# Optimization experiments

Measured on AMD Instinct MI355X. Metric: run time of the kernel, lower is better.

Reference implementation:

```python
import jax, jax.numpy as jnp
import numpy as np

B, T, D, K = 4, 4096, 1024, 64


def setup_inputs() -> dict:
    key = jax.random.key(0)
    k1, k2, k3, k4 = jax.random.split(key, 4)
    x = jax.random.normal(k1, (B, T, D), dtype=jnp.float32)
    Wq = jax.random.normal(k2, (D, K), dtype=jnp.float32) * (D ** -0.5)
    Wk = jax.random.normal(k3, (D, K), dtype=jnp.float32) * (D ** -0.5)
    Wv = jax.random.normal(k4, (D, D), dtype=jnp.float32) * (D ** -0.5)
    return {"x": x, "Wq": Wq, "Wk": Wk, "Wv": Wv}


def reference(x, Wq, Wk, Wv):
    # x: (B,T,D); single-head causal self-attention with value dim = D
    Bx, Tx, Dx = x.shape
    head_size = Wq.shape[-1]
    q = jnp.einsum('btd,dk->btk', x, Wq)  # (B,T,K)
    k = jnp.einsum('btd,dk->btk', x, Wk)  # (B,T,K)
    v = jnp.einsum('btd,de->bte', x, Wv)  # (B,T,D)
    scores = jnp.einsum('bqk,bsk->bqs', q, k) * (head_size ** -0.5)  # (B,T,T)
    causal = jnp.tril(jnp.ones((Tx, Tx), dtype=bool))
    scores = jnp.where(causal[None, :, :], scores, -jnp.inf)
    attn = jax.nn.softmax(scores, axis=-1)
    return jnp.einsum('bqs,bsd->bqd', attn, v)  # (B,T,D)
```

## Files before the change

### kernel.cpp

```cpp
#include <hip/hip_runtime.h>
#include <hip/hip_bf16.h>

typedef __attribute__((ext_vector_type(8))) short bf16x8;
typedef __attribute__((ext_vector_type(4))) float f32x4;
typedef unsigned short u16;

#define MFMA16(a, b, c) __builtin_amdgcn_mfma_f32_16x16x32_bf16((a), (b), (c), 0, 0, 0)
#define GLLDS(gp, lp)                                                                  \
  __builtin_amdgcn_global_load_lds((const __attribute__((address_space(1))) unsigned int*)(gp), \
                                   (__attribute__((address_space(3))) unsigned int*)(lp), 16, 0, 0)

__device__ __forceinline__ u16 f2b(float f) {
  union { float f; unsigned u; } x; x.f = f;
  return (u16)((x.u + 0x7FFFu + ((x.u >> 16) & 1u)) >> 16);
}
__device__ __forceinline__ u16 f2b_hw(float f) {
  union { __hip_bfloat16 h; u16 u; } c;
  c.h = __float2bfloat16(f);
  return c.u;
}

__global__ __launch_bounds__(256) void k_cvt(const float* __restrict__ in,
                                             u16* __restrict__ out, int n4) {
  int i = blockIdx.x * 256 + threadIdx.x;
  if (i >= n4) return;
  float4 v = ((const float4*)in)[i];
  u16 a = f2b(v.x), b = f2b(v.y), c = f2b(v.z), d = f2b(v.w);
  ((uint2*)out)[i] = make_uint2((unsigned)a | ((unsigned)b << 16),
                                (unsigned)c | ((unsigned)d << 16));
}

__global__ __launch_bounds__(256) void k_packT(const float* __restrict__ in,
                                               u16* __restrict__ out, int R, int C) {
  __shared__ float t[32][33];
  int r0 = blockIdx.x * 32, c0 = blockIdx.y * 32;
  int cx = threadIdx.x & 31, ry = threadIdx.x >> 5;
#pragma unroll
  for (int k = 0; k < 4; k++)
    t[ry + k * 8][cx] = in[(size_t)(r0 + ry + k * 8) * C + c0 + cx];
  __syncthreads();
#pragma unroll
  for (int k = 0; k < 4; k++)
    out[(size_t)(c0 + ry + k * 8) * R + r0 + cx] = f2b(t[cx][ry + k * 8]);
}

__global__ __launch_bounds__(256) void k_gemm_qk(const u16* __restrict__ xb,
                                                 const u16* __restrict__ wqt,
                                                 const u16* __restrict__ wkt,
                                                 u16* __restrict__ q, u16* __restrict__ kk) {
  int row0 = blockIdx.x * 64;
  int tid = threadIdx.x, w = tid >> 6, l = tid & 63, l15 = l & 15, lg = l >> 4;
  const u16* wt = (w < 2) ? wqt : wkt;
  int nbase = (w & 1) * 32;
  f32x4 acc[4][2];
#pragma unroll
  for (int mt = 0; mt < 4; mt++)
#pragma unroll
    for (int nt = 0; nt < 2; nt++) acc[mt][nt] = (f32x4){0.f, 0.f, 0.f, 0.f};

  for (int k0 = 0; k0 < 1024; k0 += 32) {
    bf16x8 bfr[2], afr[4];
#pragma unroll
    for (int nt = 0; nt < 2; nt++)
      bfr[nt] = *(const bf16x8*)&wt[(size_t)(nbase + nt * 16 + l15) * 1024 + k0 + lg * 8];
#pragma unroll
    for (int mt = 0; mt < 4; mt++)
      afr[mt] = *(const bf16x8*)&xb[(size_t)(row0 + mt * 16 + l15) * 1024 + k0 + lg * 8];
#pragma unroll
    for (int mt = 0; mt < 4; mt++)
#pragma unroll
      for (int nt = 0; nt < 2; nt++) acc[mt][nt] = MFMA16(afr[mt], bfr[nt], acc[mt][nt]);
  }
  if (w < 2) {
#pragma unroll
    for (int mt = 0; mt < 4; mt++)
#pragma unroll
      for (int nt = 0; nt < 2; nt++)
#pragma unroll
        for (int j = 0; j < 4; j++)
          q[(size_t)(row0 + mt * 16 + lg * 4 + j) * 64 + nbase + nt * 16 + l15] =
              f2b(acc[mt][nt][j] * 0.125f);
  } else {
#pragma unroll
    for (int mt = 0; mt < 4; mt++)
#pragma unroll
      for (int nt = 0; nt < 2; nt++)
#pragma unroll
        for (int j = 0; j < 4; j++) {
          int row = row0 + mt * 16 + lg * 4 + j;
          int c = (nbase + nt * 16 + l15) * 2;
          size_t off = (size_t)(row >> 6) * 8192 + (row & 63) * 128 + (c ^ ((row & 7) << 4));
          *(u16*)((char*)kk + off) = f2b(acc[mt][nt][j]);
        }
  }
}

__global__ __launch_bounds__(256) void k_gemm_v(const u16* __restrict__ xb,
                                                const u16* __restrict__ wvt,
                                                u16* __restrict__ vT) {
  int b = blockIdx.z;
  int d0 = blockIdx.y * 128;
  int s0 = blockIdx.x * 128;
  int tid = threadIdx.x, w = tid >> 6, l = tid & 63, l15 = l & 15, lg = l >> 4;
  int wd = (w & 1) * 64, wsn = (w >> 1) * 64;
  __shared__ __align__(16) char lds[32768];

  const u16* arow = wvt + (size_t)d0 * 1024;
  const u16* brow = xb + (size_t)(b * 4096 + s0) * 1024;

  auto stage = [&](int buf, int k0) {
    char* La = lds + buf * 16384;
    char* Lb = La + 8192;
#pragma unroll
    for (int i = 0; i < 2; i++) {
      int row = w * 32 + i * 16 + (l >> 2), kq = (l & 3) * 8;
      GLLDS(&arow[(size_t)row * 1024 + k0 + kq], La + (w * 2 + i) * 1024);
      GLLDS(&brow[(size_t)row * 1024 + k0 + kq], Lb + (w * 2 + i) * 1024);
    }
  };

  f32x4 acc[4][4];
#pragma unroll
  for (int mt = 0; mt < 4; mt++)
#pragma unroll
    for (int nt = 0; nt < 4; nt++) acc[mt][nt] = (f32x4){0.f, 0.f, 0.f, 0.f};

  stage(0, 0);
  __syncthreads();
  int buf = 0;
  for (int k = 0; k < 32; k++) {
    if (k < 31) stage(buf ^ 1, (k + 1) * 32);
    const char* La = lds + buf * 16384;
    const char* Lb = La + 8192;
    bf16x8 afr[4], bfr[4];
#pragma unroll
    for (int mt = 0; mt < 4; mt++)
      afr[mt] = *(const bf16x8*)(La + (wd + mt * 16 + l15) * 64 + lg * 16);
#pragma unroll
    for (int nt = 0; nt < 4; nt++)
      bfr[nt] = *(const bf16x8*)(Lb + (wsn + nt * 16 + l15) * 64 + lg * 16);
    __builtin_amdgcn_s_setprio(1);
#pragma unroll
    for (int mt = 0; mt < 4; mt++)
#pragma unroll
      for (int nt = 0; nt < 4; nt++) acc[mt][nt] = MFMA16(afr[mt], bfr[nt], acc[mt][nt]);
    __builtin_amdgcn_s_setprio(0);
    __syncthreads();
    buf ^= 1;
  }
#pragma unroll
  for (int mt = 0; mt < 4; mt++)
#pragma unroll
    for (int nt = 0; nt < 4; nt++)
#pragma unroll
      for (int j = 0; j < 4; j++) {
        int d = d0 + wd + mt * 16 + lg * 4 + j;
        int s = s0 + wsn + nt * 16 + l15;
        size_t off = ((size_t)(b * 64 + (s >> 6)) * 8 + (d >> 7)) * 16384 + (d & 127) * 128 +
                     (((s & 63) * 2) ^ ((d & 7) << 4));
        *(u16*)((char*)vT + off) = f2b(acc[mt][nt][j]);
      }
}

__global__ __launch_bounds__(512, 2) void k_attn(const u16* __restrict__ qw,
                                                 const u16* __restrict__ kws,
                                                 const u16* __restrict__ vts,
                                                 float* __restrict__ out) {
  int p = blockIdx.x, cpair = blockIdx.y, b = blockIdx.z;
  int tid = threadIdx.x, w = tid >> 6, l = tid & 63, l15 = l & 15, lg = l >> 4;
  int sw = (l15 & 7) << 4;
  size_t tokb = (size_t)b * 4096;

  __shared__ __align__(16) char lds[98816];
  char* Pb = lds + 81920;
  float* scb = (float*)(lds + 98304);

  const short ob = (short)0x3F80;
  const bf16x8 ones = {ob, ob, ob, ob, ob, ob, ob, ob};
  const bf16x8 zf = {0, 0, 0, 0, 0, 0, 0, 0};

  auto stage = [&](int t, int bufi) {
    const char* kb = (const char*)kws + (size_t)(b * 64 + t) * 8192;
    const char* vb = (const char*)vts + ((size_t)(b * 64 + t) * 8 + cpair * 2) * 16384;
    char* lk = lds + bufi * 8192;
    char* lv = lds + 16384 + bufi * 32768;
#pragma unroll
    for (int i = 0; i < 5; i++) {
      int s = w * 5 + i;
      if (s < 8) GLLDS(kb + s * 1024 + l * 16, lk + s * 1024);
      else       GLLDS(vb + (s - 8) * 1024 + l * 16, lv + (s - 8) * 1024);
    }
  };

  auto run_phase = [&](int Q0) {
    int ntb = (Q0 >> 6) + 2;
    int qsA = Q0 + w * 16;
    int qA = qsA + l15;
    int qsB = Q0 + (w & 3) * 32;
    int dhalf = w >> 2;

    bf16x8 qf[2];
#pragma unroll
    for (int ks = 0; ks < 2; ks++)
      qf[ks] = *(const bf16x8*)&qw[(tokb + qA) * 64 + ks * 32 + lg * 8];

    f32x4 acc[8][2], accl[2];
    float mrow = -1e30f;
#pragma unroll
    for (int mt = 0; mt < 8; mt++)
#pragma unroll
      for (int qt = 0; qt < 2; qt++) acc[mt][qt] = (f32x4){0.f, 0.f, 0.f, 0.f};
    accl[0] = (f32x4){0.f, 0.f, 0.f, 0.f};
    accl[1] = (f32x4){0.f, 0.f, 0.f, 0.f};

    stage(0, 0);
    asm volatile("s_waitcnt vmcnt(0)" ::: "memory");
    __builtin_amdgcn_s_barrier();
    asm volatile("" ::: "memory");
    int buf = 0;
    for (int t = 0; t < ntb; t++) {
      int s0 = t * 64;
      if (t + 1 < ntb) stage(t + 1, buf ^ 1);
      if (s0 < qsA + 16) {
        const char* Kb = lds + buf * 8192;
        f32x4 sfr[4];
        __builtin_amdgcn_s_setprio(1);
#pragma unroll
        for (int nt = 0; nt < 4; nt++) {
          const char* kr = Kb + (nt * 16 + l15) * 128;
          bf16x8 kf0 = *(const bf16x8*)(kr + ((lg * 16) ^ sw));
          bf16x8 kf1 = *(const bf16x8*)(kr + ((64 + lg * 16) ^ sw));
          f32x4 z = (f32x4){0.f, 0.f, 0.f, 0.f};
          z = MFMA16(kf0, qf[0], z);
          sfr[nt] = MFMA16(kf1, qf[1], z);
        }
        __builtin_amdgcn_s_setprio(0);
        if (s0 + 63 > qsA) {
#pragma unroll
          for (int nt = 0; nt < 4; nt++)
#pragma unroll
            for (int j = 0; j < 4; j++)
              if (s0 + nt * 16 + lg * 4 + j > qA) sfr[nt][j] = -1e30f;
        }
        float pm = fmaxf(fmaxf(fmaxf(sfr[0][0], sfr[0][1]), fmaxf(sfr[0][2], sfr[0][3])),
                         fmaxf(fmaxf(sfr[1][0], sfr[1][1]), fmaxf(sfr[1][2], sfr[1][3])));
        pm = fmaxf(pm, fmaxf(fmaxf(fmaxf(sfr[2][0], sfr[2][1]), fmaxf(sfr[2][2], sfr[2][3])),
                             fmaxf(fmaxf(sfr[3][0], sfr[3][1]), fmaxf(sfr[3][2], sfr[3][3]))));
        pm = fmaxf(pm, __shfl_xor(pm, 16));
        pm = fmaxf(pm, __shfl_xor(pm, 32));
        float sc = 1.0f;
        if (__any(pm > mrow + 8.0f)) {
          float mn = fmaxf(mrow, pm);
          sc = __expf(mrow - mn);
          mrow = mn;
        }
        int rq = w * 16 + l15;
        scb[rq] = sc;
        int rbase = rq * 128, sx = (rq & 7) << 4;
#pragma unroll
        for (int nt = 0; nt < 4; nt++) {
          unsigned lo = (unsigned)f2b_hw(__expf(sfr[nt][0] - mrow)) |
                        ((unsigned)f2b_hw(__expf(sfr[nt][1] - mrow)) << 16);
          unsigned hi = (unsigned)f2b_hw(__expf(sfr[nt][2] - mrow)) |
                        ((unsigned)f2b_hw(__expf(sfr[nt][3] - mrow)) << 16);
          int addr = (rbase + (nt * 16 + lg * 4) * 2) ^ sx;
          *(uint2*)(Pb + addr) = make_uint2(lo, hi);
        }
      }
      asm volatile("s_waitcnt lgkmcnt(0)" ::: "memory");
      __builtin_amdgcn_s_barrier();
      asm volatile("" ::: "memory");
      if (s0 < qsB + 32) {
        const char* Vb = lds + 16384 + buf * 32768 + dhalf * 16384;
        bool act0 = s0 < qsB + 16;
        int R0 = (w & 3) * 32 + l15;
        if (act0) {
          float sq0 = scb[R0];
          if (!__all(sq0 == 1.0f)) {
#pragma unroll
            for (int mt = 0; mt < 8; mt++) acc[mt][0] *= sq0;
            accl[0] *= sq0;
          }
        }
        {
          float sq1 = scb[R0 + 16];
          if (!__all(sq1 == 1.0f)) {
#pragma unroll
            for (int mt = 0; mt < 8; mt++) acc[mt][1] *= sq1;
            accl[1] *= sq1;
          }
        }
        bf16x8 pf00 = zf, pf01 = zf, pf10, pf11;
        if (act0) {
          int rx = (R0 & 7) << 4;
          pf00 = *(const bf16x8*)(Pb + ((R0 * 128 + lg * 16) ^ rx));
          pf01 = *(const bf16x8*)(Pb + ((R0 * 128 + 64 + lg * 16) ^ rx));
        }
        {
          int R1 = R0 + 16, rx = (R1 & 7) << 4;
          pf10 = *(const bf16x8*)(Pb + ((R1 * 128 + lg * 16) ^ rx));
          pf11 = *(const bf16x8*)(Pb + ((R1 * 128 + 64 + lg * 16) ^ rx));
        }
        __builtin_amdgcn_s_setprio(1);
        accl[0] = MFMA16(ones, pf00, accl[0]);
        accl[0] = MFMA16(ones, pf01, accl[0]);
        accl[1] = MFMA16(ones, pf10, accl[1]);
        accl[1] = MFMA16(ones, pf11, accl[1]);
#pragma unroll
        for (int mt = 0; mt < 8; mt++) {
          const char* vr = Vb + (mt * 16 + l15) * 128;
          bf16x8 va0 = *(const bf16x8*)(vr + ((lg * 16) ^ sw));
          bf16x8 va1 = *(const bf16x8*)(vr + ((64 + lg * 16) ^ sw));
          acc[mt][0] = MFMA16(va0, pf00, acc[mt][0]);
          acc[mt][0] = MFMA16(va1, pf01, acc[mt][0]);
          acc[mt][1] = MFMA16(va0, pf10, acc[mt][1]);
          acc[mt][1] = MFMA16(va1, pf11, acc[mt][1]);
        }
        __builtin_amdgcn_s_setprio(0);
      }
      asm volatile("s_waitcnt vmcnt(0)" ::: "memory");
      __builtin_amdgcn_s_barrier();
      asm volatile("" ::: "memory");
      buf ^= 1;
    }
#pragma unroll
    for (int qt = 0; qt < 2; qt++) {
      float linv = 1.0f / accl[qt][0];
#pragma unroll
      for (int mt = 0; mt < 8; mt++) {
        f32x4 v = acc[mt][qt] * linv;
        size_t o = (tokb + qsB + qt * 16 + l15) * 1024 + cpair * 256 + dhalf * 128 +
                   mt * 16 + lg * 4;
        *(f32x4*)&out[o] = v;
      }
    }
  };

  run_phase(p * 128);
  run_phase((31 - p) * 128);
}

extern "C" void kernel_launch(void* const* d_in, const int* in_sizes, int n_in,
                              void* d_out, int out_size, void* d_ws, size_t ws_size,
                              hipStream_t stream) {
  const float* x  = (const float*)d_in[0];
  const float* Wq = (const float*)d_in[1];
  const float* Wk = (const float*)d_in[2];
  const float* Wv = (const float*)d_in[3];
  float* out = (float*)d_out;
  char* ws = (char*)d_ws;
  u16* xb  = (u16*)(ws);
  u16* qw  = (u16*)(ws + 33554432);
  u16* kw  = (u16*)(ws + 35651584);
  u16* vT  = (u16*)(ws + 37748736);
  u16* wqt = (u16*)(ws + 71303168);
  u16* wkt = (u16*)(ws + 71434240);
  u16* wvt = (u16*)(ws + 71565312);

  k_cvt<<<16384, 256, 0, stream>>>(x, xb, 4194304);
  k_packT<<<dim3(32, 2), 256, 0, stream>>>(Wq, wqt, 1024, 64);
  k_packT<<<dim3(32, 2), 256, 0, stream>>>(Wk, wkt, 1024, 64);
  k_packT<<<dim3(32, 32), 256, 0, stream>>>(Wv, wvt, 1024, 1024);
  k_gemm_qk<<<256, 256, 0, stream>>>(xb, wqt, wkt, qw, kw);
  k_gemm_v<<<dim3(32, 8, 4), 256, 0, stream>>>(xb, wvt, vT);
  k_attn<<<dim3(16, 4, 4), 512, 0, stream>>>(qw, kw, vT, out);
}
```

Baseline: 252.6 us.

## Single-buffer V tile, shrink LDS, raise attention occupancy and remap blocks by XCD

```diff
diff --git a/kernel.cpp b/kernel.cpp
--- a/kernel.cpp
+++ b/kernel.cpp
@@ -162,34 +162,39 @@
       }
 }
 
-__global__ __launch_bounds__(512, 2) void k_attn(const u16* __restrict__ qw,
+__global__ __launch_bounds__(512, 4) void k_attn(const u16* __restrict__ qw,
                                                  const u16* __restrict__ kws,
                                                  const u16* __restrict__ vts,
                                                  float* __restrict__ out) {
-  int p = blockIdx.x, cpair = blockIdx.y, b = blockIdx.z;
+  int bid = blockIdx.x;
+  int xcd = bid & 7, rest = bid >> 3;
+  int p = rest & 15, hi = rest >> 4;
+  int g = xcd + 8 * hi;
+  int cpair = g & 3, b = g >> 2;
   int tid = threadIdx.x, w = tid >> 6, l = tid & 63, l15 = l & 15, lg = l >> 4;
   int sw = (l15 & 7) << 4;
   size_t tokb = (size_t)b * 4096;
 
-  __shared__ __align__(16) char lds[98816];
-  char* Pb = lds + 81920;
-  float* scb = (float*)(lds + 98304);
+  __shared__ __align__(16) char lds[66048];
+  char* Pb = lds + 49152;
+  float* scb = (float*)(lds + 65536);
 
   const short ob = (short)0x3F80;
   const bf16x8 ones = {ob, ob, ob, ob, ob, ob, ob, ob};
   const bf16x8 zf = {0, 0, 0, 0, 0, 0, 0, 0};
 
-  auto stage = [&](int t, int bufi) {
+  auto stageV = [&](int t) {
+    const char* vb = (const char*)vts + ((size_t)(b * 64 + t) * 8 + cpair * 2) * 16384;
+    char* lv = lds + 16384;
+#pragma unroll
+    for (int i = 0; i < 4; i++) {
+      int s = w * 4 + i;
+      GLLDS(vb + s * 1024 + l * 16, lv + s * 1024);
+    }
+  };
+  auto stageK = [&](int t, int bufi) {
     const char* kb = (const char*)kws + (size_t)(b * 64 + t) * 8192;
-    const char* vb = (const char*)vts + ((size_t)(b * 64 + t) * 8 + cpair * 2) * 16384;
-    char* lk = lds + bufi * 8192;
-    char* lv = lds + 16384 + bufi * 32768;
-#pragma unroll
-    for (int i = 0; i < 5; i++) {
-      int s = w * 5 + i;
-      if (s < 8) GLLDS(kb + s * 1024 + l * 16, lk + s * 1024);
-      else       GLLDS(vb + (s - 8) * 1024 + l * 16, lv + (s - 8) * 1024);
-    }
+    GLLDS(kb + w * 1024 + l * 16, lds + bufi * 8192 + w * 1024);
   };
 
   auto run_phase = [&](int Q0) {
@@ -213,14 +218,13 @@
     accl[0] = (f32x4){0.f, 0.f, 0.f, 0.f};
     accl[1] = (f32x4){0.f, 0.f, 0.f, 0.f};
 
-    stage(0, 0);
-    asm volatile("s_waitcnt vmcnt(0)" ::: "memory");
-    __builtin_amdgcn_s_barrier();
-    asm volatile("" ::: "memory");
+    stageK(0, 0);
+    __syncthreads();
     int buf = 0;
     for (int t = 0; t < ntb; t++) {
       int s0 = t * 64;
-      if (t + 1 < ntb) stage(t + 1, buf ^ 1);
+      stageV(t);
+      if (t + 1 < ntb) stageK(t + 1, buf ^ 1);
       if (s0 < qsA + 16) {
         const char* Kb = lds + buf * 8192;
         f32x4 sfr[4];
@@ -261,17 +265,15 @@
         for (int nt = 0; nt < 4; nt++) {
           unsigned lo = (unsigned)f2b_hw(__expf(sfr[nt][0] - mrow)) |
                         ((unsigned)f2b_hw(__expf(sfr[nt][1] - mrow)) << 16);
-          unsigned hi = (unsigned)f2b_hw(__expf(sfr[nt][2] - mrow)) |
-                        ((unsigned)f2b_hw(__expf(sfr[nt][3] - mrow)) << 16);
+          unsigned hi2 = (unsigned)f2b_hw(__expf(sfr[nt][2] - mrow)) |
+                         ((unsigned)f2b_hw(__expf(sfr[nt][3] - mrow)) << 16);
           int addr = (rbase + (nt * 16 + lg * 4) * 2) ^ sx;
-          *(uint2*)(Pb + addr) = make_uint2(lo, hi);
+          *(uint2*)(Pb + addr) = make_uint2(lo, hi2);
         }
       }
-      asm volatile("s_waitcnt lgkmcnt(0)" ::: "memory");
-      __builtin_amdgcn_s_barrier();
-      asm volatile("" ::: "memory");
+      __syncthreads();
       if (s0 < qsB + 32) {
-        const char* Vb = lds + 16384 + buf * 32768 + dhalf * 16384;
+        const char* Vb = lds + 16384 + dhalf * 16384;
         bool act0 = s0 < qsB + 16;
         int R0 = (w & 3) * 32 + l15;
         if (act0) {
@@ -318,9 +320,7 @@
         }
         __builtin_amdgcn_s_setprio(0);
       }
-      asm volatile("s_waitcnt vmcnt(0)" ::: "memory");
-      __builtin_amdgcn_s_barrier();
-      asm volatile("" ::: "memory");
+      __syncthreads();
       buf ^= 1;
     }
 #pragma unroll
@@ -363,5 +363,5 @@
   k_packT<<<dim3(32, 32), 256, 0, stream>>>(Wv, wvt, 1024, 1024);
   k_gemm_qk<<<256, 256, 0, stream>>>(xb, wqt, wkt, qw, kw);
   k_gemm_v<<<dim3(32, 8, 4), 256, 0, stream>>>(xb, wvt, vT);
-  k_attn<<<dim3(16, 4, 4), 512, 0, stream>>>(qw, kw, vT, out);
-}
+  k_attn<<<256, 512, 0, stream>>>(qw, kw, vT, out);
+}
```

After: 291.8 us. +15.5%, slower.
